# Kernel optimization log

Measured on AMD Instinct MI355X. Metric: run time of the kernel, lower is better.

## Reference

```python
import jax, jax.numpy as jnp
import numpy as np

B, S, HID = 2, 2048, 1024
H, KV, D = 16, 8, 64
NDIM = 2          # position_ids.shape[-1]
EPS = 1e-6
SCALING = 1.0


def _rms_norm(x, w=None, eps=EPS):
    # matches _RMSNorm: fp32 compute, optional learnable scale
    xf = x.astype(jnp.float32)
    n = xf * jax.lax.rsqrt(jnp.mean(xf * xf, axis=-1, keepdims=True) + eps)
    if w is not None:
        n = n * w.astype(jnp.float32)
    return n.astype(x.dtype)


def _rotate_half(x):
    d = x.shape[-1] // 2
    return jnp.concatenate([-x[..., d:], x[..., :d]], axis=-1)


def _apply_multidim_rope(x, cos, sin, ndim):
    # x: [B,S,h,D]; cos/sin: [B,S,D]; unsqueeze_dim=2 broadcasts over heads
    num_channels = x.shape[-1]
    cpd = 2 * (num_channels // (2 * ndim))  # channels per RoPE dimension
    outs = []
    for k in range(ndim):
        sl = slice(k * cpd, (k + 1) * cpd)
        xk = x[..., sl]
        ck = cos[..., sl][:, :, None, :]
        sk = sin[..., sl][:, :, None, :]
        outs.append(xk * ck + _rotate_half(xk) * sk)
    return jnp.concatenate(outs, axis=-1)


def setup_inputs() -> dict:
    key = jax.random.key(0)
    ks = jax.random.split(key, 10)
    scale = 0.02
    return {
        "hidden_states": jax.random.normal(ks[0], (B, S, HID), jnp.float32),
        "cos": jax.random.normal(ks[1], (B, S, D), jnp.float32),
        "sin": jax.random.normal(ks[2], (B, S, D), jnp.float32),
        "position_ids": jax.random.randint(ks[3], (B, S, NDIM), 0, 64, jnp.int64),
        "Wq": jax.random.normal(ks[4], (HID, H * D), jnp.float32) * scale,
        "Wk": jax.random.normal(ks[5], (HID, KV * D), jnp.float32) * scale,
        "Wv": jax.random.normal(ks[6], (HID, KV * D), jnp.float32) * scale,
        "Wo": jax.random.normal(ks[7], (H * D, HID), jnp.float32) * scale,
        "q_norm_w": jnp.ones((D,), jnp.float32),
        "k_norm_w": jnp.ones((D,), jnp.float32),
    }


def reference(hidden_states, cos, sin, position_ids, Wq, Wk, Wv, Wo, q_norm_w, k_norm_w):
    ndim = position_ids.shape[-1]
    bsz, seq_len, _ = hidden_states.shape

    q = (hidden_states @ Wq).reshape(bsz, seq_len, H, D)
    q = _rms_norm(q, q_norm_w)
    q = _apply_multidim_rope(q, cos, sin, ndim)
    q = jnp.transpose(q, (0, 2, 1, 3))  # [B,H,S,D]

    k = (hidden_states @ Wk).reshape(bsz, seq_len, KV, D)
    k = _rms_norm(k, k_norm_w)
    k = _apply_multidim_rope(k, cos, sin, ndim)
    k = jnp.transpose(k, (0, 2, 1, 3))  # [B,KV,S,D]

    v = (hidden_states @ Wv).reshape(bsz, seq_len, KV, D)
    v = _rms_norm(v, None)  # v_norm has no scale
    v = jnp.transpose(v, (0, 2, 1, 3))  # [B,KV,S,D]

    groups = H // KV
    if groups > 1:
        k = jnp.repeat(k, groups, axis=1)  # [B,H,S,D]
        v = jnp.repeat(v, groups, axis=1)

    scores = jnp.einsum("bhqd,bhkd->bhqk", q, k) * SCALING
    attn = jax.nn.softmax(scores.astype(jnp.float32), axis=-1).astype(q.dtype)
    out = jnp.einsum("bhqk,bhkd->bhqd", attn, v)
    out = jnp.transpose(out, (0, 2, 1, 3)).reshape(bsz, seq_len, H * D)
    return out @ Wo
```

## Files before the change

### kernel.cpp

```cpp
#include <hip/hip_runtime.h>

#define PB 2
#define PS 2048
#define PHID 1024
#define PH 16
#define PKV 8
#define PD 64
#define PM (PB*PS)
#define PR (PB*PH*PS)

typedef _Float16 f16_t;
typedef _Float16 f16x8 __attribute__((ext_vector_type(8)));
typedef _Float16 f16x2 __attribute__((ext_vector_type(2)));
typedef float f32x4 __attribute__((ext_vector_type(4)));

#define MFMAH(a,b,c)  __builtin_amdgcn_mfma_f32_16x16x32_f16((a),(b),(c),0,0,0)
#define LOG2E 1.44269504f

__device__ __forceinline__ void gl16(const f16_t* g, f16_t* l) {
  __builtin_amdgcn_global_load_lds(
      (const __attribute__((address_space(1))) void*)g,
      (__attribute__((address_space(3))) void*)l, 16, 0, 0);
}

__global__ __launch_bounds__(256)
void convert_hs(const float* __restrict__ hs, f16_t* __restrict__ hf)
{
  const size_t i = ((size_t)blockIdx.x * 256 + threadIdx.x) * 8;
  float4 a = *(const float4*)&hs[i];
  float4 b = *(const float4*)&hs[i + 4];
  float xs[8] = {a.x, a.y, a.z, a.w, b.x, b.y, b.z, b.w};
  f16x8 v;
  #pragma unroll
  for (int j = 0; j < 8; ++j) v[j] = (f16_t)xs[j];
  *(f16x8*)&hf[i] = v;
}

__global__ __launch_bounds__(256)
void convert_w(const float* __restrict__ Wq, const float* __restrict__ Wk,
               const float* __restrict__ Wv, const float* __restrict__ Wo,
               f16_t* __restrict__ wtT)
{
  __shared__ float Tt[64][68];
  const int tid = threadIdx.x;
  const int slot = blockIdx.x >> 4, k0 = (blockIdx.x & 15) * 64;

  const float* src; int N, ncol0, orow0;
  if (slot < 16)      { src = Wq; N = 1024; ncol0 = slot*64;      orow0 = slot*64; }
  else if (slot < 24) { src = Wk; N = 512;  ncol0 = (slot-16)*64; orow0 = 1024 + (slot-16)*64; }
  else if (slot < 32) { src = Wv; N = 512;  ncol0 = (slot-24)*64; orow0 = 1536 + (slot-24)*64; }
  else                { src = Wo; N = 1024; ncol0 = (slot-32)*64; orow0 = 2048 + (slot-32)*64; }

  const int tk = tid >> 6, tn = tid & 63;
  #pragma unroll
  for (int i = 0; i < 16; ++i)
    Tt[tn][tk*16 + i] = src[(size_t)(k0 + tk*16 + i) * N + ncol0 + tn];
  __syncthreads();

  const int n = tid >> 2, kc = (tid & 3) * 16;
  f16x8 a0, a1;
  #pragma unroll
  for (int i = 0; i < 8; ++i) {
    a0[i] = (f16_t)Tt[n][kc + i];
    a1[i] = (f16_t)Tt[n][kc + 8 + i];
  }
  const size_t ob = (size_t)(orow0 + n) * 1024 + k0 + kc;
  *(f16x8*)&wtT[ob]     = a0;
  *(f16x8*)&wtT[ob + 8] = a1;
}

__global__ __launch_bounds__(256)
void qkv_kernel(const f16_t* __restrict__ hsf, const f16_t* __restrict__ wtT,
                const float* __restrict__ cosp, const float* __restrict__ sinp,
                const float* __restrict__ qnw, const float* __restrict__ knw,
                f16_t* __restrict__ q_o, f16_t* __restrict__ k_o,
                f16_t* __restrict__ vt_o)
{
  __shared__ __align__(16) f16_t Ah[128][64];
  __shared__ __align__(16) f16_t Bh[128][64];

  const int tid = threadIdx.x;
  const int lane = tid & 63, wave = tid >> 6;
  const int lo16 = lane & 15, hi4 = lane >> 4;
  const int lin = blockIdx.x;
  const int swz = (lin & 7) * 64 + (lin >> 3);
  const int m0 = (swz >> 4) * 128;
  const int ws = swz & 15;
  const int orow = ws * 128;

  int kind, hd0;
  if (ws < 8)       { kind = 0; hd0 = ws*2; }
  else if (ws < 12) { kind = 1; hd0 = (ws-8)*2; }
  else              { kind = 2; hd0 = (ws-12)*2; }

  f32x4 acc[2][8];
  #pragma unroll
  for (int qb = 0; qb < 2; ++qb)
    #pragma unroll
    for (int j = 0; j < 8; ++j) acc[qb][j] = f32x4{0.f, 0.f, 0.f, 0.f};

  const int ri = lane >> 3, pc = lane & 7;
  const int lcs = (pc ^ ri) * 8;
  size_t aoff4[4]; f16_t* aldst4[4];
  size_t boff4[4]; f16_t* bldst4[4];
  #pragma unroll
  for (int q = 0; q < 4; ++q) {
    aoff4[q] = (size_t)(m0 + wave*32 + q*8 + ri) * PHID + lcs;
    aldst4[q] = &Ah[wave*32 + q*8][0];
    boff4[q] = (size_t)(orow + wave*32 + q*8 + ri) * 1024 + lcs;
    bldst4[q] = &Bh[wave*32 + q*8][0];
  }

  const int rsw = lo16 & 7;

  for (int k0 = 0; k0 < PHID; k0 += 64) {
    __syncthreads();
    #pragma unroll
    for (int q = 0; q < 4; ++q) gl16(hsf + aoff4[q] + k0, aldst4[q]);
    #pragma unroll
    for (int q = 0; q < 4; ++q) gl16(wtT + boff4[q] + k0, bldst4[q]);
    __syncthreads();

    #pragma unroll
    for (int t = 0; t < 2; ++t) {
      const int ccol = ((t*4 + hi4) ^ rsw) * 8;
      f16x8 ah[2];
      #pragma unroll
      for (int qb = 0; qb < 2; ++qb)
        ah[qb] = *(const f16x8*)&Ah[wave*32 + qb*16 + lo16][ccol];
      #pragma unroll
      for (int j = 0; j < 8; ++j) {
        f16x8 bh = *(const f16x8*)&Bh[j*16 + lo16][ccol];
        #pragma unroll
        for (int qb = 0; qb < 2; ++qb)
          acc[qb][j] = MFMAH(ah[qb], bh, acc[qb][j]);
      }
    }
  }

  float nwv[4];
  #pragma unroll
  for (int jj = 0; jj < 4; ++jj)
    nwv[jj] = (kind == 0) ? qnw[lo16 + 16*jj]
            : (kind == 1) ? knw[lo16 + 16*jj] : 1.0f;

  #pragma unroll
  for (int qb = 0; qb < 2; ++qb) {
    float sc[2][4];
    #pragma unroll
    for (int r = 0; r < 4; ++r) {
      float s0 = 0.f, s1 = 0.f;
      #pragma unroll
      for (int j = 0; j < 4; ++j) {
        s0 += acc[qb][j][r]   * acc[qb][j][r];
        s1 += acc[qb][j+4][r] * acc[qb][j+4][r];
      }
      #pragma unroll
      for (int m = 1; m < 16; m <<= 1) {
        s0 += __shfl_xor(s0, m);
        s1 += __shfl_xor(s1, m);
      }
      sc[0][r] = 1.0f / sqrtf(s0 * (1.0f/64.0f) + 1e-6f);
      sc[1][r] = 1.0f / sqrtf(s1 * (1.0f/64.0f) + 1e-6f);
    }

    float y[8][4];
    #pragma unroll
    for (int j = 0; j < 8; ++j)
      #pragma unroll
      for (int r = 0; r < 4; ++r)
        y[j][r] = acc[qb][j][r] * sc[j>>2][r] * nwv[j&3];

    if (kind == 2) {
      #pragma unroll
      for (int r = 0; r < 4; ++r) {
        int mg = m0 + wave*32 + qb*16 + hi4*4 + r;
        int b = mg >> 11, sq = mg & 2047;
        int g = sq & 63;
        int sp = (g & 3) | (((g >> 4) & 1) << 2) | (((g >> 2) & 1) << 3)
               | (((g >> 3) & 1) << 4) | (g & 32);
        int sq2 = (sq & ~63) | sp;
        #pragma unroll
        for (int j = 0; j < 8; ++j) {
          int d = lo16 + 16*(j & 3), hd = hd0 + (j >> 2);
          vt_o[((size_t)((b*PKV + hd)*PD + d))*PS + sq2] = (f16_t)y[j][r];
        }
      }
    } else {
      #pragma unroll
      for (int r = 0; r < 4; ++r) {
        int mg = m0 + wave*32 + qb*16 + hi4*4 + r;
        int b = mg >> 11, sq = mg & 2047;
        const float* cp = &cosp[(size_t)mg * PD];
        const float* sp = &sinp[(size_t)mg * PD];
        float z[8];
        #pragma unroll
        for (int j = 0; j < 8; ++j) {
          int d = lo16 + 16*(j & 3);
          float c = cp[d], s = sp[d];
          float rot = (j & 1) ? y[j-1][r] : -y[j+1][r];
          z[j] = y[j][r] * c + rot * s;
        }
        #pragma unroll
        for (int j = 0; j < 8; ++j) {
          int d = lo16 + 16*(j & 3), hd = hd0 + (j >> 2);
          if (kind == 0) {
            size_t idx = ((size_t)(b*PH + hd)*PS + sq)*PD + d;
            q_o[idx] = (f16_t)(z[j] * LOG2E);
          } else {
            size_t idx = ((size_t)(b*PKV + hd)*PS + sq)*PD + d;
            k_o[idx] = (f16_t)z[j];
          }
        }
      }
    }
  }
}

__global__ __launch_bounds__(256, 4)
void attn_kernel(const f16_t* __restrict__ q_g, const f16_t* __restrict__ k_g,
                 const f16_t* __restrict__ vt_g,
                 f16_t* __restrict__ op, float2* __restrict__ ml)
{
  __shared__ __align__(16) char lds_raw[32768];
  f16_t (*Ks)[64][64] = (f16_t (*)[64][64])lds_raw;
  f16_t (*Vs)[64][64] = (f16_t (*)[64][64])(lds_raw + 16384);
  f16_t (*Ob)[72]     = (f16_t (*)[72])lds_raw;

  const int tid = threadIdx.x, lane = tid & 63, wave = tid >> 6;
  const int lo16 = lane & 15, hi4 = lane >> 4;
  const int lin = blockIdx.x;
  const int swz = (lin & 7) * 128 + (lin >> 3);
  const int qt = swz & 15;
  const int bh = (swz >> 4) & 31;
  const int ks = swz >> 9;
  const int b = bh >> 4, h = bh & 15, kvh = h >> 1;

  f16x8 qf[2][2];
  #pragma unroll
  for (int qb = 0; qb < 2; ++qb) {
    const size_t qbase = ((size_t)(b*PH + h)*PS + qt*128 + wave*32 + qb*16 + lo16) * PD;
    #pragma unroll
    for (int t = 0; t < 2; ++t)
      qf[qb][t] = *(const f16x8*)&q_g[qbase + t*32 + hi4*8];
  }

  f32x4 o[2][4];
  float mq[2] = {-1e30f, -1e30f}, lq[2] = {0.f, 0.f};
  #pragma unroll
  for (int qb = 0; qb < 2; ++qb)
    #pragma unroll
    for (int j = 0; j < 4; ++j) o[qb][j] = f32x4{0.f, 0.f, 0.f, 0.f};

  const f32x4 FZ = {0.f, 0.f, 0.f, 0.f};

  const int ri = lane >> 3;
  const int lcs = ((lane & 7) ^ ri) * 8;
  const size_t kbase = (size_t)(b*PKV + kvh) * PS * PD + (size_t)ks * 1024 * PD;
  const size_t vbase = (size_t)(b*PKV + kvh) * PD * PS + (size_t)ks * 1024;

  auto STAGE = [&](int kt, int buf) {
    const f16_t* kp = k_g + kbase + (size_t)kt * 64 * PD;
    const f16_t* vp = vt_g + vbase + kt * 64;
    #pragma unroll
    for (int i = 0; i < 2; ++i) {
      const int st = wave*2 + i;
      gl16(kp + (st*8 + ri)*PD + lcs, &Ks[buf][st*8][0]);
      gl16(vp + (size_t)(st*8 + ri)*PS + lcs, &Vs[buf][st*8][0]);
    }
  };

  STAGE(0, 0);
  int cur = 0;
  const int rsw = lo16 & 7;

  for (int kt = 0; kt < 16; ++kt) {
    __syncthreads();
    if (kt + 1 < 16) STAGE(kt + 1, cur ^ 1);

    f32x4 sacc[2][4];
    __builtin_amdgcn_s_setprio(1);
    #pragma unroll
    for (int j = 0; j < 4; ++j) {
      f16x8 kf0 = *(const f16x8*)&Ks[cur][j*16 + lo16][(hi4 ^ rsw) * 8];
      f16x8 kf1 = *(const f16x8*)&Ks[cur][j*16 + lo16][((4 + hi4) ^ rsw) * 8];
      #pragma unroll
      for (int qb = 0; qb < 2; ++qb)
        sacc[qb][j] = MFMAH(kf1, qf[qb][1], MFMAH(kf0, qf[qb][0], FZ));
    }
    __builtin_amdgcn_s_setprio(0);

    f16x8 pa[2][2];
    #pragma unroll
    for (int qb = 0; qb < 2; ++qb) {
      float x0 = fmaxf(fmaxf(sacc[qb][0][0], sacc[qb][0][1]),
                       fmaxf(sacc[qb][0][2], sacc[qb][0][3]));
      float x1 = fmaxf(fmaxf(sacc[qb][1][0], sacc[qb][1][1]),
                       fmaxf(sacc[qb][1][2], sacc[qb][1][3]));
      float x2 = fmaxf(fmaxf(sacc[qb][2][0], sacc[qb][2][1]),
                       fmaxf(sacc[qb][2][2], sacc[qb][2][3]));
      float x3 = fmaxf(fmaxf(sacc[qb][3][0], sacc[qb][3][1]),
                       fmaxf(sacc[qb][3][2], sacc[qb][3][3]));
      float tm = fmaxf(fmaxf(x0, x1), fmaxf(x2, x3));
      tm = fmaxf(tm, __shfl_xor(tm, 16));
      tm = fmaxf(tm, __shfl_xor(tm, 32));
      if (!__all(tm <= mq[qb] + 8.0f)) {
        float mnew = fmaxf(mq[qb], tm);
        float alpha = __builtin_amdgcn_exp2f(mq[qb] - mnew);
        lq[qb] *= alpha;
        #pragma unroll
        for (int jd = 0; jd < 4; ++jd) o[qb][jd] *= alpha;
        mq[qb] = mnew;
      }
      float ls = 0.f;
      #pragma unroll
      for (int t = 0; t < 2; ++t) {
        f16x8 v;
        #pragma unroll
        for (int e = 0; e < 8; ++e) {
          float p = __builtin_amdgcn_exp2f(sacc[qb][2*t + (e >> 2)][e & 3] - mq[qb]);
          ls += p;
          v[e] = (f16_t)p;
        }
        pa[qb][t] = v;
      }
      ls += __shfl_xor(ls, 16);
      ls += __shfl_xor(ls, 32);
      lq[qb] += ls;
    }

    __builtin_amdgcn_s_setprio(1);
    #pragma unroll
    for (int jd = 0; jd < 4; ++jd) {
      #pragma unroll
      for (int t = 0; t < 2; ++t) {
        f16x8 vf = *(const f16x8*)&Vs[cur][jd*16 + lo16][((t*4 + hi4) ^ rsw) * 8];
        #pragma unroll
        for (int qb = 0; qb < 2; ++qb)
          o[qb][jd] = MFMAH(vf, pa[qb][t], o[qb][jd]);
      }
    }
    __builtin_amdgcn_s_setprio(0);

    cur ^= 1;
  }

  __syncthreads();
  const int rbase = bh*PS + qt*128 + wave*32;
  if (hi4 == 0) {
    #pragma unroll
    for (int qb = 0; qb < 2; ++qb)
      ml[(size_t)ks*PR + rbase + qb*16 + lo16] = float2{mq[qb], lq[qb]};
  }
  #pragma unroll
  for (int qb = 0; qb < 2; ++qb) {
    float inv = 1.0f / lq[qb];
    #pragma unroll
    for (int jd = 0; jd < 4; ++jd)
      #pragma unroll
      for (int rp = 0; rp < 2; ++rp)
        *(f16x2*)&Ob[wave*32 + qb*16 + lo16][jd*16 + hi4*4 + 2*rp] =
            f16x2{(f16_t)(o[qb][jd][2*rp] * inv), (f16_t)(o[qb][jd][2*rp+1] * inv)};
  }
  {
    const int row = lane >> 1, half = lane & 1;
    const size_t gb_ = ((size_t)ks*PR + rbase + row) * PD + half*32;
    #pragma unroll
    for (int c = 0; c < 4; ++c)
      *(f16x8*)&op[gb_ + c*8] = *(const f16x8*)&Ob[wave*32 + row][half*32 + c*8];
  }
}

__global__ __launch_bounds__(256)
void merge_kernel(const f16_t* __restrict__ op, const float2* __restrict__ ml,
                  f16_t* __restrict__ ao)
{
  const int gid = blockIdx.x * 256 + threadIdx.x;
  const int row = gid >> 3, oct = gid & 7;
  float2 e0 = ml[row], e1 = ml[PR + row];
  float M = fmaxf(e0.x, e1.x);
  float c0 = __builtin_amdgcn_exp2f(e0.x - M) * e0.y;
  float c1 = __builtin_amdgcn_exp2f(e1.x - M) * e1.y;
  float inv = 1.0f / (c0 + c1);
  c0 *= inv; c1 *= inv;
  f16x8 a = *(const f16x8*)&op[(size_t)row*PD + oct*8];
  f16x8 bq = *(const f16x8*)&op[(size_t)(PR + row)*PD + oct*8];
  f16x8 r;
  #pragma unroll
  for (int i = 0; i < 8; ++i)
    r[i] = (f16_t)(c0 * (float)a[i] + c1 * (float)bq[i]);
  const int bh = row >> 11, sq = row & 2047;
  const int b = bh >> 4, h = bh & 15;
  *(f16x8*)&ao[((size_t)(b*PS + sq))*PHID + h*PD + oct*8] = r;
}

__global__ __launch_bounds__(256)
void oproj_kernel(const f16_t* __restrict__ ao, const f16_t* __restrict__ woT,
                  float* __restrict__ out)
{
  __shared__ __align__(16) f16_t As[128][64];
  __shared__ __align__(16) f16_t Bs[64][64];

  const int tid = threadIdx.x;
  const int lane = tid & 63, wave = tid >> 6;
  const int lo16 = lane & 15, hi4 = lane >> 4;
  const int lin = blockIdx.x;
  const int swz = (lin & 7) * 64 + (lin >> 3);
  const int m0 = (swz >> 4) * 128;
  const int col0 = (swz & 15) * 64;

  f32x4 acc[2][4];
  #pragma unroll
  for (int qb = 0; qb < 2; ++qb)
    #pragma unroll
    for (int j = 0; j < 4; ++j) acc[qb][j] = f32x4{0.f, 0.f, 0.f, 0.f};

  const int ri = lane >> 3, pc = lane & 7;
  const int lcs = (pc ^ ri) * 8;
  size_t aoff4[4]; f16_t* aldst4[4];
  #pragma unroll
  for (int q = 0; q < 4; ++q) {
    aoff4[q] = (size_t)(m0 + wave*32 + q*8 + ri) * PHID + lcs;
    aldst4[q] = &As[wave*32 + q*8][0];
  }
  size_t boff[2]; int brow[2];
  #pragma unroll
  for (int q = 0; q < 2; ++q) {
    brow[q] = wave*16 + q*8;
    boff[q] = (size_t)(col0 + brow[q] + ri) * 1024 + lcs;
  }

  const int rsw = lo16 & 7;

  for (int k0 = 0; k0 < PHID; k0 += 64) {
    __syncthreads();
    #pragma unroll
    for (int q = 0; q < 4; ++q) gl16(ao + aoff4[q] + k0, aldst4[q]);
    #pragma unroll
    for (int q = 0; q < 2; ++q) gl16(woT + boff[q] + k0, &Bs[brow[q]][0]);
    __syncthreads();

    #pragma unroll
    for (int t = 0; t < 2; ++t) {
      const int ccol = ((t*4 + hi4) ^ rsw) * 8;
      f16x8 a[2];
      #pragma unroll
      for (int qb = 0; qb < 2; ++qb)
        a[qb] = *(const f16x8*)&As[wave*32 + qb*16 + lo16][ccol];
      #pragma unroll
      for (int j = 0; j < 4; ++j) {
        f16x8 bb = *(const f16x8*)&Bs[j*16 + lo16][ccol];
        #pragma unroll
        for (int qb = 0; qb < 2; ++qb)
          acc[qb][j] = MFMAH(a[qb], bb, acc[qb][j]);
      }
    }
  }

  #pragma unroll
  for (int qb = 0; qb < 2; ++qb)
    #pragma unroll
    for (int r = 0; r < 4; ++r) {
      int mg = m0 + wave*32 + qb*16 + hi4*4 + r;
      #pragma unroll
      for (int j = 0; j < 4; ++j)
        out[(size_t)mg*PHID + col0 + lo16 + 16*j] = acc[qb][j][r];
    }
}

extern "C" void kernel_launch(void* const* d_in, const int* in_sizes, int n_in,
                              void* d_out, int out_size, void* d_ws, size_t ws_size,
                              hipStream_t stream) {
  (void)in_sizes; (void)n_in; (void)out_size; (void)ws_size;
  const float* hs   = (const float*)d_in[0];
  const float* cosp = (const float*)d_in[1];
  const float* sinp = (const float*)d_in[2];
  const float* Wq   = (const float*)d_in[4];
  const float* Wk   = (const float*)d_in[5];
  const float* Wv   = (const float*)d_in[6];
  const float* Wo   = (const float*)d_in[7];
  const float* qnw  = (const float*)d_in[8];
  const float* knw  = (const float*)d_in[9];
  float* out = (float*)d_out;

  const size_t QN = (size_t)PB*PH*PS*PD;
  const size_t KN = (size_t)PB*PKV*PS*PD;
  const size_t HN = (size_t)PM*PHID;
  char* wsb = (char*)d_ws;
  f16_t*  qv  = (f16_t*)wsb;
  f16_t*  kv  = qv + QN;
  f16_t*  vt  = kv + KN;
  f16_t*  hsf = vt + KN;
  f16_t*  wtT = hsf + HN;
  f16_t*  op  = wtT + (size_t)3072*1024;
  float2* ml  = (float2*)(op + 2*QN);
  f16_t*  ao  = qv;
  const f16_t* woT = wtT + (size_t)2048*1024;

  convert_hs<<<dim3(2048), 256, 0, stream>>>(hs, hsf);
  convert_w <<<dim3(768),  256, 0, stream>>>(Wq, Wk, Wv, Wo, wtT);
  qkv_kernel<<<dim3(512),  256, 0, stream>>>(hsf, wtT, cosp, sinp,
                                             qnw, knw, qv, kv, vt);
  attn_kernel<<<dim3(1024), 256, 0, stream>>>(qv, kv, vt, op, ml);
  merge_kernel<<<dim3(PR*8/256), 256, 0, stream>>>(op, ml, ao);
  oproj_kernel<<<dim3(512), 256, 0, stream>>>(ao, woT, out);
}
```

Measured before the change: 117.5 us.

## Merge conversion kernels and defer softmax row-sum reductions out of attention loop

Combines the hidden-state and weight fp32->fp16 conversion kernels into one launch, removing one kernel launch and its tail. In the attention inner loop, probabilities are packed with cvt_pkrtz, which converts two values per instruction but rounds toward zero. The cross-lane shuffle reduction of the row sum is moved from every iteration to once after the loop. Deferring the sum stays correct because every lane is rescaled by the same alpha, at the cost of slightly different rounding.

```diff
diff --git a/kernel.cpp b/kernel.cpp
--- a/kernel.cpp
+++ b/kernel.cpp
@@ -12,6 +12,7 @@
 typedef _Float16 f16_t;
 typedef _Float16 f16x8 __attribute__((ext_vector_type(8)));
 typedef _Float16 f16x2 __attribute__((ext_vector_type(2)));
+typedef __fp16 fp16v2 __attribute__((ext_vector_type(2)));
 typedef float f32x4 __attribute__((ext_vector_type(4)));
 
 #define MFMAH(a,b,c)  __builtin_amdgcn_mfma_f32_16x16x32_f16((a),(b),(c),0,0,0)
@@ -24,26 +25,28 @@
 }
 
 __global__ __launch_bounds__(256)
-void convert_hs(const float* __restrict__ hs, f16_t* __restrict__ hf)
-{
-  const size_t i = ((size_t)blockIdx.x * 256 + threadIdx.x) * 8;
-  float4 a = *(const float4*)&hs[i];
-  float4 b = *(const float4*)&hs[i + 4];
-  float xs[8] = {a.x, a.y, a.z, a.w, b.x, b.y, b.z, b.w};
-  f16x8 v;
-  #pragma unroll
-  for (int j = 0; j < 8; ++j) v[j] = (f16_t)xs[j];
-  *(f16x8*)&hf[i] = v;
-}
-
-__global__ __launch_bounds__(256)
-void convert_w(const float* __restrict__ Wq, const float* __restrict__ Wk,
-               const float* __restrict__ Wv, const float* __restrict__ Wo,
-               f16_t* __restrict__ wtT)
+void convert_all(const float* __restrict__ hs,
+                 const float* __restrict__ Wq, const float* __restrict__ Wk,
+                 const float* __restrict__ Wv, const float* __restrict__ Wo,
+                 f16_t* __restrict__ hf, f16_t* __restrict__ wtT)
 {
   __shared__ float Tt[64][68];
   const int tid = threadIdx.x;
-  const int slot = blockIdx.x >> 4, k0 = (blockIdx.x & 15) * 64;
+
+  if (blockIdx.x < 2048) {
+    const size_t i = ((size_t)blockIdx.x * 256 + tid) * 8;
+    float4 a = *(const float4*)&hs[i];
+    float4 b = *(const float4*)&hs[i + 4];
+    float xs[8] = {a.x, a.y, a.z, a.w, b.x, b.y, b.z, b.w};
+    f16x8 v;
+    #pragma unroll
+    for (int j = 0; j < 8; ++j) v[j] = (f16_t)xs[j];
+    *(f16x8*)&hf[i] = v;
+    return;
+  }
+
+  const int wb = blockIdx.x - 2048;
+  const int slot = wb >> 4, k0 = (wb & 15) * 64;
 
   const float* src; int N, ncol0, orow0;
   if (slot < 16)      { src = Wq; N = 1024; ncol0 = slot*64;      orow0 = slot*64; }
@@ -315,17 +318,16 @@
       float ls = 0.f;
       #pragma unroll
       for (int t = 0; t < 2; ++t) {
-        f16x8 v;
-        #pragma unroll
-        for (int e = 0; e < 8; ++e) {
-          float p = __builtin_amdgcn_exp2f(sacc[qb][2*t + (e >> 2)][e & 3] - mq[qb]);
-          ls += p;
-          v[e] = (f16_t)p;
+        union { fp16v2 h[4]; f16x8 v; } u;
+        #pragma unroll
+        for (int pr = 0; pr < 4; ++pr) {
+          float p0 = __builtin_amdgcn_exp2f(sacc[qb][2*t + (pr>>1)][(pr&1)*2]     - mq[qb]);
+          float p1 = __builtin_amdgcn_exp2f(sacc[qb][2*t + (pr>>1)][(pr&1)*2 + 1] - mq[qb]);
+          ls += p0 + p1;
+          u.h[pr] = __builtin_amdgcn_cvt_pkrtz(p0, p1);
         }
-        pa[qb][t] = v;
-      }
-      ls += __shfl_xor(ls, 16);
-      ls += __shfl_xor(ls, 32);
+        pa[qb][t] = u.v;
+      }
       lq[qb] += ls;
     }
 
@@ -345,6 +347,11 @@
     cur ^= 1;
   }
 
+  #pragma unroll
+  for (int qb = 0; qb < 2; ++qb) {
+    lq[qb] += __shfl_xor(lq[qb], 16);
+    lq[qb] += __shfl_xor(lq[qb], 32);
+  }
   __syncthreads();
   const int rbase = bh*PS + qt*128 + wave*32;
   if (hi4 == 0) {
@@ -497,8 +504,7 @@
   f16_t*  ao  = qv;
   const f16_t* woT = wtT + (size_t)2048*1024;
 
-  convert_hs<<<dim3(2048), 256, 0, stream>>>(hs, hsf);
-  convert_w <<<dim3(768),  256, 0, stream>>>(Wq, Wk, Wv, Wo, wtT);
+  convert_all<<<dim3(2816), 256, 0, stream>>>(hs, Wq, Wk, Wv, Wo, hsf, wtT);
   qkv_kernel<<<dim3(512),  256, 0, stream>>>(hsf, wtT, cosp, sinp,
                                              qnw, knw, qv, kv, vt);
   attn_kernel<<<dim3(1024), 256, 0, stream>>>(qv, kv, vt, op, ml);
```

After: 115.9 us. About the same (-1.4%).
